# Kernel optimization log

Hardware: AMD Instinct MI355X
Metric: run time of the kernel (lower is better)

The kernel has to match this reference:

```python
import jax, jax.numpy as jnp
import numpy as np
import math

B = 16; L = 1024; CIN = 3; COUT = 1; D = 128; K = 16; DEPTH = 4
EPS = 1e-5; GRID_RANGE = 1.0


def _haar_basis(L):
    # Orthonormal Haar wavelet basis, rows of V (L, L). L must be power of 2.
    V = np.zeros((L, L), dtype=np.float64)
    V[0, :] = 1.0 / math.sqrt(L)
    r, s = 1, 1
    while s < L and r < L:
        block = 2 * s
        amp = 1.0 / math.sqrt(block)
        for j in range(L // block):
            st = j * block
            V[r, st:st + s] = amp
            V[r, st + s:st + block] = -amp
            r += 1
            if r >= L:
                break
        s *= 2
    return V


def _phi_f(L, k):
    # rFFT of top-k Haar basis rows, complex64 (matches build_stu_basis_rfft)
    V = _haar_basis(L)
    return jnp.asarray(np.fft.rfft(V, axis=-1)[:k].astype(np.complex64))


def setup_inputs() -> dict:
    key = jax.random.key(0)
    ks = jax.random.split(key, 8)

    def rn(k, shape, scale):
        return jax.random.normal(k, shape, dtype=jnp.float32) * scale

    return {
        "x": jax.random.normal(ks[0], (B, CIN, L), dtype=jnp.float32),
        "lift_w": rn(ks[1], (D, CIN + 1), 1.0 / math.sqrt(CIN + 1)),  # conv1x1 weight
        "lift_b": jnp.zeros((D,), jnp.float32),
        "Phi_f": _phi_f(L, K),                                        # (K, L//2+1) complex64 buffer
        "theta": rn(ks[2], (DEPTH, K, D, D), 1.0 / math.sqrt(D)),
        "ln_g": jnp.ones((DEPTH, D), jnp.float32),
        "ln_b": jnp.zeros((DEPTH, D), jnp.float32),
        "fc1_w": rn(ks[3], (DEPTH, 2 * D, D), 1.0 / math.sqrt(D)),
        "fc1_b": jnp.zeros((DEPTH, 2 * D), jnp.float32),
        "fc2_w": rn(ks[4], (DEPTH, D, 2 * D), 1.0 / math.sqrt(2 * D)),
        "fc2_b": jnp.zeros((DEPTH, D), jnp.float32),
        "head_w": rn(ks[5], (COUT, D), 1.0 / math.sqrt(D)),
        "head_b": jnp.zeros((COUT,), jnp.float32),
    }


def _forward(x, lift_w, lift_b, Phi_f, theta, ln_g, ln_b,
             fc1_w, fc1_b, fc2_w, fc2_b, head_w, head_b):
    # add_grid: append linspace coord channel -> (B, CIN+1, L)
    coords = jnp.linspace(0.0, GRID_RANGE, L, dtype=x.dtype)
    coords = jnp.broadcast_to(coords, (x.shape[0], 1, L))
    xg = jnp.concatenate([x, coords], axis=1)

    # LocalLift1D with kernel_size=1 == pointwise linear over channels
    h = jnp.einsum('bcl,dc->bdl', xg, lift_w) + lift_b[None, :, None]

    Phic = jnp.conj(Phi_f)  # (K, Lr)
    for i in range(DEPTH):
        # LayerNorm over channel dim (torch LN on transposed (B,L,D))
        mu = jnp.mean(h, axis=1, keepdims=True)
        var = jnp.var(h, axis=1, keepdims=True)
        z = (h - mu) / jnp.sqrt(var + EPS) * ln_g[i][None, :, None] + ln_b[i][None, :, None]

        Xf = jnp.fft.rfft(z, axis=-1)                       # (B, D, Lr)
        Uf = Xf[:, :, None, :] * Phic[None, None, :, :]     # (B, D, K, Lr)
        U = jnp.fft.irfft(Uf, n=L, axis=-1)                 # (B, D, K, L)

        # fused einsum('bdln,lhd->bhln') + sum over l(=k)
        S = jnp.einsum('bdkn,khd->bhn', U, theta[i])        # (B, D, L)

        # pointwise MLP (conv1x1 -> GELU -> conv1x1), residual
        H1 = jax.nn.gelu(jnp.einsum('bdl,hd->bhl', S, fc1_w[i]) + fc1_b[i][None, :, None],
                         approximate=False)
        h = h + jnp.einsum('bhl,dh->bdl', H1, fc2_w[i]) + fc2_b[i][None, :, None]

    # head: conv1x1 lifting_dim -> out_dim
    return jnp.einsum('bdl,od->bol', h, head_w) + head_b[None, :, None]


def reference(x, lift_w, lift_b, Phi_f, theta, ln_g, ln_b,
              fc1_w, fc1_b, fc2_w, fc2_b, head_w, head_b):
    return _forward(x, lift_w, lift_b, Phi_f, theta, ln_g, ln_b,
                    fc1_w, fc1_b, fc2_w, fc2_b, head_w, head_b)
```

## Files before the change

### kernel.cpp

```cpp
#include <hip/hip_runtime.h>
#include <math.h>

#define BB 16
#define LL 1024
#define DD 128
#define BL (BB*LL)
#define NDEPTH 4
#define EPSF 1e-5f

typedef unsigned short u16;
typedef short bf16x8 __attribute__((ext_vector_type(8)));
typedef short bf16x4 __attribute__((ext_vector_type(4)));
typedef float f32x4 __attribute__((ext_vector_type(4)));

static __device__ __forceinline__ u16 f2bf(float x) {
    unsigned u = __float_as_uint(x);
    u = u + 0x7fffu + ((u >> 16) & 1u);
    return (u16)(u >> 16);
}

#define DZ_B 0
#define S_B  15360
#define H1_B 23552
#define RST_B 39936
#define MRS_B 40064
#define LDS_TOT 40192

#define N_TH (4*15*16384)
#define N_W1 (4*32768)
#define N_W2 (4*32768)
__global__ __launch_bounds__(256) void cvt_kernel(const float* __restrict__ theta,
        const float* __restrict__ fc1w, const float* __restrict__ fc2w,
        u16* __restrict__ thf, u16* __restrict__ w1f, u16* __restrict__ w2f) {
    int o = blockIdx.x * 256 + threadIdx.x;
    if (o < N_TH) {
        int j = o & 7, ln = (o >> 3) & 63, c = (o >> 9) & 3, f = (o >> 11) & 7;
        int slab = o >> 14;
        int layer = slab / 15, kk = slab - layer * 15;
        int h = f * 16 + (ln & 15), d = 32 * c + 8 * (ln >> 4) + j;
        thf[o] = f2bf(theta[(((size_t)layer * 16 + kk + 1) * 128 + h) * 128 + d]);
    } else if (o < N_TH + N_W1) {
        int o2 = o - N_TH;
        int j = o2 & 7, ln = (o2 >> 3) & 63, c = (o2 >> 9) & 3, f = (o2 >> 11) & 15;
        int layer = o2 >> 15;
        int m = f * 16 + (ln & 15), d = 32 * c + 8 * (ln >> 4) + j;
        w1f[o2] = f2bf(fc1w[(size_t)layer * 32768 + m * 128 + d]);
    } else if (o < N_TH + N_W1 + N_W2) {
        int o2 = o - (N_TH + N_W1);
        int j = o2 & 7, ln = (o2 >> 3) & 63, c = (o2 >> 9) & 7, f = (o2 >> 12) & 7;
        int layer = o2 >> 15;
        int d = f * 16 + (ln & 15), m = 32 * c + 8 * (ln >> 4) + j;
        w2f[o2] = f2bf(fc2w[(size_t)layer * 32768 + d * 256 + m]);
    }
}

__global__ __launch_bounds__(512) void prep0_kernel(const float* __restrict__ x,
        const float* __restrict__ lw, const float* __restrict__ lb,
        float* __restrict__ H, float2* __restrict__ stats,
        float* __restrict__ P1p, float* __restrict__ P2p) {
    __shared__ char lds[16384 + 256];
    float* rst = (float*)(lds + 16384);
    float* mrs = (float*)(lds + 16384 + 128);
    int b = blockIdx.y, nblk = blockIdx.x, t0 = nblk * 32, tid = threadIdx.x;

    #pragma unroll
    for (int it = 0; it < 2; ++it) {
        int idx = it * 512 + tid;
        int r = idx >> 5, d0 = (idx & 31) * 4;
        int l = t0 + r;
        float x0 = x[(size_t)b * 3072 + l];
        float x1 = x[(size_t)b * 3072 + 1024 + l];
        float x2 = x[(size_t)b * 3072 + 2048 + l];
        float coord = (float)l * (1.0f / 1023.0f);
        f32x4 hv;
        #pragma unroll
        for (int q = 0; q < 4; ++q) {
            int d = d0 + q;
            float4 w = *(const float4*)(lw + d * 4);
            hv[q] = lb[d] + w.x * x0 + w.y * x1 + w.z * x2 + w.w * coord;
        }
        *(f32x4*)(H + ((size_t)b * 1024 + l) * 128 + d0) = hv;
        int byte = r * 512 + ((d0 * 4) ^ ((r & 7) << 4));
        *(f32x4*)(lds + byte) = hv;
    }
    __syncthreads();
    {
        int t = tid >> 4, q = tid & 15;
        float s = 0.f, sq = 0.f;
        #pragma unroll
        for (int dd = 0; dd < 8; dd += 4) {
            int d = q * 8 + dd;
            int byte = t * 512 + ((d * 4) ^ ((t & 7) << 4));
            f32x4 v = *(const f32x4*)(lds + byte);
            s += v[0] + v[1] + v[2] + v[3];
            sq += v[0]*v[0] + v[1]*v[1] + v[2]*v[2] + v[3]*v[3];
        }
        #pragma unroll
        for (int o = 1; o < 16; o <<= 1) {
            s += __shfl_xor(s, o, 64); sq += __shfl_xor(sq, o, 64);
        }
        if (q == 0) {
            float mu = s * (1.f / 128.f);
            float var = sq * (1.f / 128.f) - mu * mu;
            float rs = rsqrtf(var + EPSF);
            stats[(size_t)b * 1024 + t0 + t] = make_float2(mu, rs);
            rst[t] = rs; mrs[t] = mu * rs;
        }
    }
    __syncthreads();
    if (tid < 128) {
        float s = 0.f;
        #pragma unroll 8
        for (int t = 0; t < 32; ++t) {
            int byte = t * 512 + ((tid * 4) ^ ((t & 7) << 4));
            s += *(const float*)(lds + byte) * rst[t];
        }
        P1p[((size_t)b * 32 + nblk) * 128 + tid] = s;
    } else if (tid == 128) {
        float s = 0.f;
        for (int t = 0; t < 32; ++t) s += mrs[t];
        P2p[b * 32 + nblk] = s;
    }
}

__global__ __launch_bounds__(128) void c_kernel(const float* __restrict__ theta0,
        const float* __restrict__ P1p, const float* __restrict__ P2p,
        const float* __restrict__ lng, const float* __restrict__ lnb,
        float* __restrict__ C) {
    __shared__ float zsum[128];
    int b = blockIdx.x, hc = blockIdx.y, tid = threadIdx.x;
    float s = 0.f;
    #pragma unroll 8
    for (int j = 0; j < 32; ++j) s += P1p[((size_t)b * 32 + j) * 128 + tid];
    float p2 = 0.f;
    #pragma unroll 8
    for (int j = 0; j < 32; ++j) p2 += P2p[b * 32 + j];
    zsum[tid] = lng[tid] * (s - p2) + 1024.0f * lnb[tid];
    __syncthreads();
    int h = hc * 16 + (tid >> 3), q = tid & 7;
    const float* th = theta0 + h * 128 + q * 16;
    float acc = 0.f;
    #pragma unroll
    for (int d = 0; d < 16; d += 4) {
        float4 tv = *(const float4*)(th + d);
        acc += tv.x * zsum[q*16 + d] + tv.y * zsum[q*16 + d + 1]
             + tv.z * zsum[q*16 + d + 2] + tv.w * zsum[q*16 + d + 3];
    }
    acc += __shfl_xor(acc, 1, 64);
    acc += __shfl_xor(acc, 2, 64);
    acc += __shfl_xor(acc, 4, 64);
    if (q == 0) C[b * 128 + h] = acc * (1.0f / 32.0f);
}

template<int LAST>
__global__ __launch_bounds__(512, 4) void mega_kernel(
        const float* __restrict__ Hin, const float2* __restrict__ stin,
        const float* __restrict__ lng,
        const u16* __restrict__ thf, const float* __restrict__ Cb_,
        const u16* __restrict__ w1f, const float* __restrict__ b1,
        const u16* __restrict__ w2f, const float* __restrict__ b2,
        float* __restrict__ Hout, float2* __restrict__ stout,
        float* __restrict__ P1p, float* __restrict__ P2p,
        const float* __restrict__ hwp, const float* __restrict__ hbp,
        float* __restrict__ out) {
    __shared__ char lds[LDS_TOT];
    int b = blockIdx.y, nblk = blockIdx.x, n0 = nblk * 32, tid = threadIdx.x;
    const float inv_s2 = 0.70710678118654752f;

    const float* Hb = Hin + (size_t)b * 1024 * 128;
    const float2* stb = stin + (size_t)b * 1024;
    for (int c = tid; c < 60 * 16; c += 512) {
        int r = c >> 4, d0 = (c & 15) * 8;
        int gr = (n0 + r) & 1023, g1 = (n0 + r + 1) & 1023;
        const float* ha = Hb + (size_t)gr * 128 + d0;
        const float* hc = Hb + (size_t)g1 * 128 + d0;
        float2 sa = stb[gr], sb = stb[g1];
        u16 tmp[8];
        #pragma unroll
        for (int j = 0; j < 8; ++j) {
            float za = (ha[j] - sa.x) * sa.y;
            float zc = (hc[j] - sb.x) * sb.y;
            tmp[j] = f2bf((za - zc) * inv_s2 * lng[d0 + j]);
        }
        int byte = r * 256 + ((d0 * 2) ^ ((r & 7) << 4));
        *(bf16x8*)(lds + byte) = *(bf16x8*)tmp;
    }
    __syncthreads();

    int wave = tid >> 6, lane = tid & 63;
    int lm = lane & 15, lk = (lane >> 4) * 8;
    int fb = (wave & 3) * 2;
    int tw0 = (wave >> 2) * 16;
    f32x4 zero4 = {0.f, 0.f, 0.f, 0.f};

    f32x4 accS[2] = {zero4, zero4};
    {
        const u16* thl = thf + (size_t)lane * 8;
        #pragma unroll 4
        for (int it = 0; it < 60; ++it) {
            int kk = it >> 2, c4 = it & 3;
            bf16x8 afr0 = *(const bf16x8*)(thl + ((size_t)((kk * 8 + fb + 0) * 4 + c4) << 9));
            bf16x8 afr1 = *(const bf16x8*)(thl + ((size_t)((kk * 8 + fb + 1) * 4 + c4) << 9));
            int trow = tw0 + lm + 2 * kk;
            int byte = trow * 256 + (((c4 * 32 + lk) * 2) ^ ((trow & 7) << 4));
            bf16x8 bfr = *(const bf16x8*)(lds + byte);
            accS[0] = __builtin_amdgcn_mfma_f32_16x16x32_bf16(afr0, bfr, accS[0], 0, 0, 0);
            accS[1] = __builtin_amdgcn_mfma_f32_16x16x32_bf16(afr1, bfr, accS[1], 0, 0, 0);
        }
    }

    {
        const float* Crow = Cb_ + b * 128;
        int tl = tw0 + lm;
        #pragma unroll
        for (int mt = 0; mt < 2; ++mt) {
            int h0 = (fb + mt) * 16 + (lane >> 4) * 4;
            f32x4 cv = *(const f32x4*)(Crow + h0);
            u16 o[4];
            #pragma unroll
            for (int r = 0; r < 4; ++r) o[r] = f2bf(accS[mt][r] + cv[r]);
            int byte = S_B + tl * 256 + ((h0 * 2) ^ ((tl & 7) << 4));
            *(bf16x4*)(lds + byte) = *(bf16x4*)o;
        }
    }
    __syncthreads();

    {
        f32x4 acc1[2][2];
        #pragma unroll
        for (int mt = 0; mt < 2; ++mt)
            #pragma unroll
            for (int nt = 0; nt < 2; ++nt) acc1[mt][nt] = zero4;
        const u16* w1l = w1f + (size_t)lane * 8;
        #pragma unroll
        for (int c4 = 0; c4 < 4; ++c4) {
            bf16x8 afr[2], bfr[2];
            #pragma unroll
            for (int mt = 0; mt < 2; ++mt)
                afr[mt] = *(const bf16x8*)(w1l + ((size_t)((wave * 2 + mt) * 4 + c4) << 9));
            #pragma unroll
            for (int nt = 0; nt < 2; ++nt) {
                int tl = nt * 16 + lm;
                int byte = S_B + tl * 256 + (((c4 * 32 + lk) * 2) ^ ((tl & 7) << 4));
                bfr[nt] = *(const bf16x8*)(lds + byte);
            }
            #pragma unroll
            for (int mt = 0; mt < 2; ++mt)
                #pragma unroll
                for (int nt = 0; nt < 2; ++nt)
                    acc1[mt][nt] = __builtin_amdgcn_mfma_f32_16x16x32_bf16(
                        afr[mt], bfr[nt], acc1[mt][nt], 0, 0, 0);
        }
        #pragma unroll
        for (int mt = 0; mt < 2; ++mt) {
            int mo = wave * 32 + mt * 16 + (lane >> 4) * 4;
            f32x4 bb4 = *(const f32x4*)(b1 + mo);
            #pragma unroll
            for (int nt = 0; nt < 2; ++nt) {
                int tl = nt * 16 + lm;
                u16 o[4];
                #pragma unroll
                for (int r = 0; r < 4; ++r) {
                    float xv = acc1[mt][nt][r] + bb4[r];
                    o[r] = f2bf(0.5f * xv * (1.0f + erff(xv * 0.70710678118654752f)));
                }
                int byte = H1_B + tl * 512 + ((mo * 2) ^ ((tl & 7) << 4));
                *(bf16x4*)(lds + byte) = *(bf16x4*)o;
            }
        }
    }
    __syncthreads();

    f32x4 acc2[2] = {zero4, zero4};
    {
        const u16* w2l = w2f + (size_t)lane * 8;
        #pragma unroll
        for (int c8 = 0; c8 < 8; ++c8) {
            bf16x8 afr = *(const bf16x8*)(w2l + ((size_t)(wave * 8 + c8) << 9));
            #pragma unroll
            for (int nt = 0; nt < 2; ++nt) {
                int tl = nt * 16 + lm;
                int byte = H1_B + tl * 512 + (((c8 * 32 + lk) * 2) ^ ((tl & 7) << 4));
                bf16x8 bfr = *(const bf16x8*)(lds + byte);
                acc2[nt] = __builtin_amdgcn_mfma_f32_16x16x32_bf16(afr, bfr, acc2[nt], 0, 0, 0);
            }
        }
    }
    __syncthreads();

    {
        int dbase = wave * 16 + (lane >> 4) * 4;
        #pragma unroll
        for (int nt = 0; nt < 2; ++nt) {
            int tl = nt * 16 + lm;
            int byte = H1_B + tl * 512 + ((dbase * 4) ^ ((tl & 7) << 4));
            *(f32x4*)(lds + byte) = acc2[nt];
        }
    }
    __syncthreads();

    {
        const float* Hrow = Hin + ((size_t)b * 1024 + n0) * 128;
        float* Horow = Hout + ((size_t)b * 1024 + n0) * 128;
        #pragma unroll
        for (int it = 0; it < 2; ++it) {
            int idx = it * 512 + tid;
            int r = idx >> 5, d0 = (idx & 31) * 4;
            int byte = H1_B + r * 512 + ((d0 * 4) ^ ((r & 7) << 4));
            f32x4 v = *(const f32x4*)(lds + byte);
            f32x4 bb = *(const f32x4*)(b2 + d0);
            f32x4 hv = *(const f32x4*)(Hrow + (size_t)r * 128 + d0);
            hv = hv + v + bb;
            if (LAST) {
                f32x4 wv = *(const f32x4*)(hwp + d0);
                float s = hv[0]*wv[0] + hv[1]*wv[1] + hv[2]*wv[2] + hv[3]*wv[3];
                #pragma unroll
                for (int o = 1; o < 32; o <<= 1) s += __shfl_xor(s, o, 64);
                if ((lane & 31) == 0) out[(size_t)b * 1024 + n0 + r] = s + hbp[0];
            } else {
                *(f32x4*)(Horow + (size_t)r * 128 + d0) = hv;
                *(f32x4*)(lds + byte) = hv;
            }
        }
    }
    if (!LAST) {
        __syncthreads();
        float* rst = (float*)(lds + RST_B);
        float* mrs = (float*)(lds + MRS_B);
        {
            int t = tid >> 4, q = tid & 15;
            float s = 0.f, sq = 0.f;
            #pragma unroll
            for (int dd = 0; dd < 8; dd += 4) {
                int d = q * 8 + dd;
                int byte = H1_B + t * 512 + ((d * 4) ^ ((t & 7) << 4));
                f32x4 v = *(const f32x4*)(lds + byte);
                s += v[0] + v[1] + v[2] + v[3];
                sq += v[0]*v[0] + v[1]*v[1] + v[2]*v[2] + v[3]*v[3];
            }
            #pragma unroll
            for (int o = 1; o < 16; o <<= 1) {
                s += __shfl_xor(s, o, 64); sq += __shfl_xor(sq, o, 64);
            }
            if (q == 0) {
                float mu = s * (1.f / 128.f);
                float var = sq * (1.f / 128.f) - mu * mu;
                float rs = rsqrtf(var + EPSF);
                stout[(size_t)b * 1024 + n0 + t] = make_float2(mu, rs);
                rst[t] = rs; mrs[t] = mu * rs;
            }
        }
        __syncthreads();
        if (tid < 128) {
            float s = 0.f;
            #pragma unroll 8
            for (int t = 0; t < 32; ++t) {
                int byte = H1_B + t * 512 + ((tid * 4) ^ ((t & 7) << 4));
                s += *(const float*)(lds + byte) * rst[t];
            }
            P1p[((size_t)b * 32 + nblk) * 128 + tid] = s;
        } else if (tid == 128) {
            float s = 0.f;
            for (int t = 0; t < 32; ++t) s += mrs[t];
            P2p[b * 32 + nblk] = s;
        }
    }
}

extern "C" void kernel_launch(void* const* d_in, const int* in_sizes, int n_in,
                              void* d_out, int out_size, void* d_ws, size_t ws_size,
                              hipStream_t stream) {
    const float* x     = (const float*)d_in[0];
    const float* lw    = (const float*)d_in[1];
    const float* lb    = (const float*)d_in[2];
    const float* theta = (const float*)d_in[4];
    const float* ln_g  = (const float*)d_in[5];
    const float* ln_b  = (const float*)d_in[6];
    const float* fc1w  = (const float*)d_in[7];
    const float* fc1b  = (const float*)d_in[8];
    const float* fc2w  = (const float*)d_in[9];
    const float* fc2b  = (const float*)d_in[10];
    const float* hw    = (const float*)d_in[11];
    const float* hb    = (const float*)d_in[12];

    float* ws = (float*)d_ws;
    float* H_A = ws;
    float* H_B = H_A + (size_t)BL * DD;
    float2* st_A = (float2*)(H_B + (size_t)BL * DD);
    float2* st_B = st_A + BL;
    float* P1p = (float*)(st_B + BL);
    float* P2p = P1p + 16 * 32 * 128;
    float* Cb  = P2p + 512;
    u16* thf = (u16*)(Cb + 2048);
    u16* w1f = thf + N_TH;
    u16* w2f = w1f + N_W1;

    cvt_kernel<<<(N_TH + N_W1 + N_W2) / 256, 256, 0, stream>>>(theta, fc1w, fc2w, thf, w1f, w2f);
    prep0_kernel<<<dim3(32, 16), 512, 0, stream>>>(x, lw, lb, H_A, st_A, P1p, P2p);

    float* Hi = H_A; float* Ho = H_B;
    float2* sti = st_A; float2* sto = st_B;
    for (int i = 0; i < NDEPTH; ++i) {
        c_kernel<<<dim3(16, 8), 128, 0, stream>>>(theta + (size_t)i * 16 * 16384, P1p, P2p,
                                                  ln_g + i * 128, ln_b + i * 128, Cb);
        if (i < NDEPTH - 1) {
            mega_kernel<0><<<dim3(32, 16), 512, 0, stream>>>(
                Hi, sti, ln_g + i * 128,
                thf + (size_t)i * 15 * 16384, Cb,
                w1f + (size_t)i * 32768, fc1b + i * 256,
                w2f + (size_t)i * 32768, fc2b + i * 128,
                Ho, sto, P1p, P2p, hw, hb, (float*)d_out);
        } else {
            mega_kernel<1><<<dim3(32, 16), 512, 0, stream>>>(
                Hi, sti, ln_g + i * 128,
                thf + (size_t)i * 15 * 16384, Cb,
                w1f + (size_t)i * 32768, fc1b + i * 256,
                w2f + (size_t)i * 32768, fc2b + i * 128,
                Ho, sto, P1p, P2p, hw, hb, (float*)d_out);
        }
        float* tH = Hi; Hi = Ho; Ho = tH;
        float2* tS = sti; sti = sto; sto = tS;
    }
}
```

Before: 141.0 us.

## Fuse per-layer C bias kernel into mega kernel and restructure theta MFMA loop

Removes the separate c_kernel launch per layer. Each mega_kernel block now reduces the P1/P2 partials itself and computes the k=0 theta bias vector into LDS, using a bf16 copy of theta0 made in cvt_kernel. To avoid a read/write race, the P1/P2 partial buffers are double-buffered across layers. The spectral MFMA loop is also remapped so each wave owns 16 output channels across both 16-token tiles, with theta fragments double-buffered in registers. The cost is redundant C computation in every block and a bf16 rounding of theta0.

```diff
diff --git a/kernel.cpp b/kernel.cpp
--- a/kernel.cpp
+++ b/kernel.cpp
@@ -18,20 +18,27 @@
     u = u + 0x7fffu + ((u >> 16) & 1u);
     return (u16)(u >> 16);
 }
-
-#define DZ_B 0
-#define S_B  15360
-#define H1_B 23552
-#define RST_B 39936
-#define MRS_B 40064
-#define LDS_TOT 40192
+static __device__ __forceinline__ float bf2f(short v) {
+    return __uint_as_float(((unsigned)(unsigned short)v) << 16);
+}
+
+#define DZ_B  0
+#define S_B   15360
+#define H1_B  23552
+#define ZS_B  39936
+#define C_B   40448
+#define RST_B 40960
+#define MRS_B 41088
+#define LDS_TOT 41216
 
 #define N_TH (4*15*16384)
 #define N_W1 (4*32768)
 #define N_W2 (4*32768)
+#define N_TH0 (4*16384)
 __global__ __launch_bounds__(256) void cvt_kernel(const float* __restrict__ theta,
         const float* __restrict__ fc1w, const float* __restrict__ fc2w,
-        u16* __restrict__ thf, u16* __restrict__ w1f, u16* __restrict__ w2f) {
+        u16* __restrict__ thf, u16* __restrict__ w1f, u16* __restrict__ w2f,
+        u16* __restrict__ th0f) {
     int o = blockIdx.x * 256 + threadIdx.x;
     if (o < N_TH) {
         int j = o & 7, ln = (o >> 3) & 63, c = (o >> 9) & 3, f = (o >> 11) & 7;
@@ -51,6 +58,10 @@
         int layer = o2 >> 15;
         int d = f * 16 + (ln & 15), m = 32 * c + 8 * (ln >> 4) + j;
         w2f[o2] = f2bf(fc2w[(size_t)layer * 32768 + d * 256 + m]);
+    } else if (o < N_TH + N_W1 + N_W2 + N_TH0) {
+        int o2 = o - (N_TH + N_W1 + N_W2);
+        int layer = o2 >> 14, idx = o2 & 16383;
+        th0f[o2] = f2bf(theta[(size_t)layer * 262144 + idx]);
     }
 }
 
@@ -123,44 +134,16 @@
     }
 }
 
-__global__ __launch_bounds__(128) void c_kernel(const float* __restrict__ theta0,
-        const float* __restrict__ P1p, const float* __restrict__ P2p,
-        const float* __restrict__ lng, const float* __restrict__ lnb,
-        float* __restrict__ C) {
-    __shared__ float zsum[128];
-    int b = blockIdx.x, hc = blockIdx.y, tid = threadIdx.x;
-    float s = 0.f;
-    #pragma unroll 8
-    for (int j = 0; j < 32; ++j) s += P1p[((size_t)b * 32 + j) * 128 + tid];
-    float p2 = 0.f;
-    #pragma unroll 8
-    for (int j = 0; j < 32; ++j) p2 += P2p[b * 32 + j];
-    zsum[tid] = lng[tid] * (s - p2) + 1024.0f * lnb[tid];
-    __syncthreads();
-    int h = hc * 16 + (tid >> 3), q = tid & 7;
-    const float* th = theta0 + h * 128 + q * 16;
-    float acc = 0.f;
-    #pragma unroll
-    for (int d = 0; d < 16; d += 4) {
-        float4 tv = *(const float4*)(th + d);
-        acc += tv.x * zsum[q*16 + d] + tv.y * zsum[q*16 + d + 1]
-             + tv.z * zsum[q*16 + d + 2] + tv.w * zsum[q*16 + d + 3];
-    }
-    acc += __shfl_xor(acc, 1, 64);
-    acc += __shfl_xor(acc, 2, 64);
-    acc += __shfl_xor(acc, 4, 64);
-    if (q == 0) C[b * 128 + h] = acc * (1.0f / 32.0f);
-}
-
 template<int LAST>
 __global__ __launch_bounds__(512, 4) void mega_kernel(
         const float* __restrict__ Hin, const float2* __restrict__ stin,
-        const float* __restrict__ lng,
-        const u16* __restrict__ thf, const float* __restrict__ Cb_,
+        const float* __restrict__ lng, const float* __restrict__ lnb,
+        const u16* __restrict__ thf, const u16* __restrict__ th0f,
         const u16* __restrict__ w1f, const float* __restrict__ b1,
         const u16* __restrict__ w2f, const float* __restrict__ b2,
         float* __restrict__ Hout, float2* __restrict__ stout,
-        float* __restrict__ P1p, float* __restrict__ P2p,
+        const float* __restrict__ P1in, const float* __restrict__ P2in,
+        float* __restrict__ P1out, float* __restrict__ P2out,
         const float* __restrict__ hwp, const float* __restrict__ hbp,
         float* __restrict__ out) {
     __shared__ char lds[LDS_TOT];
@@ -185,40 +168,96 @@
         int byte = r * 256 + ((d0 * 2) ^ ((r & 7) << 4));
         *(bf16x8*)(lds + byte) = *(bf16x8*)tmp;
     }
+    if (tid < 128) {
+        float s = 0.f;
+        #pragma unroll 8
+        for (int j = 0; j < 32; ++j) s += P1in[((size_t)b * 32 + j) * 128 + tid];
+        float p2 = 0.f;
+        #pragma unroll 8
+        for (int j = 0; j < 32; ++j) p2 += P2in[b * 32 + j];
+        ((float*)(lds + ZS_B))[tid] = lng[tid] * (s - p2) + 1024.0f * lnb[tid];
+    }
     __syncthreads();
 
     int wave = tid >> 6, lane = tid & 63;
     int lm = lane & 15, lk = (lane >> 4) * 8;
-    int fb = (wave & 3) * 2;
-    int tw0 = (wave >> 2) * 16;
     f32x4 zero4 = {0.f, 0.f, 0.f, 0.f};
 
+    {
+        int h = tid >> 2, q = tid & 3;
+        const u16* th0 = th0f + h * 128 + q * 32;
+        const float* zs = (const float*)(lds + ZS_B) + q * 32;
+        float acc = 0.f;
+        #pragma unroll
+        for (int c = 0; c < 4; ++c) {
+            bf16x8 tv = *(const bf16x8*)(th0 + c * 8);
+            #pragma unroll
+            for (int j = 0; j < 8; ++j) acc += bf2f(tv[j]) * zs[c * 8 + j];
+        }
+        acc += __shfl_xor(acc, 1, 64);
+        acc += __shfl_xor(acc, 2, 64);
+        if (q == 0) ((float*)(lds + C_B))[h] = acc * (1.0f / 32.0f);
+    }
+    __syncthreads();
+
     f32x4 accS[2] = {zero4, zero4};
     {
-        const u16* thl = thf + (size_t)lane * 8;
-        #pragma unroll 4
-        for (int it = 0; it < 60; ++it) {
-            int kk = it >> 2, c4 = it & 3;
-            bf16x8 afr0 = *(const bf16x8*)(thl + ((size_t)((kk * 8 + fb + 0) * 4 + c4) << 9));
-            bf16x8 afr1 = *(const bf16x8*)(thl + ((size_t)((kk * 8 + fb + 1) * 4 + c4) << 9));
-            int trow = tw0 + lm + 2 * kk;
-            int byte = trow * 256 + (((c4 * 32 + lk) * 2) ^ ((trow & 7) << 4));
-            bf16x8 bfr = *(const bf16x8*)(lds + byte);
-            accS[0] = __builtin_amdgcn_mfma_f32_16x16x32_bf16(afr0, bfr, accS[0], 0, 0, 0);
-            accS[1] = __builtin_amdgcn_mfma_f32_16x16x32_bf16(afr1, bfr, accS[1], 0, 0, 0);
-        }
-    }
-
-    {
-        const float* Crow = Cb_ + b * 128;
-        int tl = tw0 + lm;
-        #pragma unroll
-        for (int mt = 0; mt < 2; ++mt) {
-            int h0 = (fb + mt) * 16 + (lane >> 4) * 4;
-            f32x4 cv = *(const f32x4*)(Crow + h0);
+        const u16* thl = thf + (size_t)lane * 8 + (size_t)wave * 2048;
+        bf16x8 bufA[4], bufB[4];
+        #pragma unroll
+        for (int c4 = 0; c4 < 4; ++c4)
+            bufA[c4] = *(const bf16x8*)(thl + c4 * 512);
+        #pragma unroll
+        for (int kp = 0; kp < 7; ++kp) {
+            int kk = kp * 2;
+            #pragma unroll
+            for (int c4 = 0; c4 < 4; ++c4)
+                bufB[c4] = *(const bf16x8*)(thl + (size_t)(kk + 1) * 16384 + c4 * 512);
+            #pragma unroll
+            for (int c4 = 0; c4 < 4; ++c4) {
+                #pragma unroll
+                for (int nt = 0; nt < 2; ++nt) {
+                    int trow = nt * 16 + lm + 2 * kk;
+                    int byte = trow * 256 + (((c4 * 32 + lk) * 2) ^ ((trow & 7) << 4));
+                    bf16x8 bfr = *(const bf16x8*)(lds + byte);
+                    accS[nt] = __builtin_amdgcn_mfma_f32_16x16x32_bf16(bufA[c4], bfr, accS[nt], 0, 0, 0);
+                }
+            }
+            #pragma unroll
+            for (int c4 = 0; c4 < 4; ++c4)
+                bufA[c4] = *(const bf16x8*)(thl + (size_t)(kk + 2) * 16384 + c4 * 512);
+            #pragma unroll
+            for (int c4 = 0; c4 < 4; ++c4) {
+                #pragma unroll
+                for (int nt = 0; nt < 2; ++nt) {
+                    int trow = nt * 16 + lm + 2 * (kk + 1);
+                    int byte = trow * 256 + (((c4 * 32 + lk) * 2) ^ ((trow & 7) << 4));
+                    bf16x8 bfr = *(const bf16x8*)(lds + byte);
+                    accS[nt] = __builtin_amdgcn_mfma_f32_16x16x32_bf16(bufB[c4], bfr, accS[nt], 0, 0, 0);
+                }
+            }
+        }
+        #pragma unroll
+        for (int c4 = 0; c4 < 4; ++c4) {
+            #pragma unroll
+            for (int nt = 0; nt < 2; ++nt) {
+                int trow = nt * 16 + lm + 28;
+                int byte = trow * 256 + (((c4 * 32 + lk) * 2) ^ ((trow & 7) << 4));
+                bf16x8 bfr = *(const bf16x8*)(lds + byte);
+                accS[nt] = __builtin_amdgcn_mfma_f32_16x16x32_bf16(bufA[c4], bfr, accS[nt], 0, 0, 0);
+            }
+        }
+    }
+
+    {
+        int h0 = wave * 16 + (lane >> 4) * 4;
+        f32x4 cv = *(const f32x4*)(lds + C_B + h0 * 4);
+        #pragma unroll
+        for (int nt = 0; nt < 2; ++nt) {
+            int tl = nt * 16 + lm;
             u16 o[4];
             #pragma unroll
-            for (int r = 0; r < 4; ++r) o[r] = f2bf(accS[mt][r] + cv[r]);
+            for (int r = 0; r < 4; ++r) o[r] = f2bf(accS[nt][r] + cv[r]);
             int byte = S_B + tl * 256 + ((h0 * 2) ^ ((tl & 7) << 4));
             *(bf16x4*)(lds + byte) = *(bf16x4*)o;
         }
@@ -358,11 +397,11 @@
                 int byte = H1_B + t * 512 + ((tid * 4) ^ ((t & 7) << 4));
                 s += *(const float*)(lds + byte) * rst[t];
             }
-            P1p[((size_t)b * 32 + nblk) * 128 + tid] = s;
+            P1out[((size_t)b * 32 + nblk) * 128 + tid] = s;
         } else if (tid == 128) {
             float s = 0.f;
             for (int t = 0; t < 32; ++t) s += mrs[t];
-            P2p[b * 32 + nblk] = s;
+            P2out[b * 32 + nblk] = s;
         }
     }
 }
@@ -388,37 +427,43 @@
     float* H_B = H_A + (size_t)BL * DD;
     float2* st_A = (float2*)(H_B + (size_t)BL * DD);
     float2* st_B = st_A + BL;
-    float* P1p = (float*)(st_B + BL);
-    float* P2p = P1p + 16 * 32 * 128;
-    float* Cb  = P2p + 512;
-    u16* thf = (u16*)(Cb + 2048);
-    u16* w1f = thf + N_TH;
-    u16* w2f = w1f + N_W1;
-
-    cvt_kernel<<<(N_TH + N_W1 + N_W2) / 256, 256, 0, stream>>>(theta, fc1w, fc2w, thf, w1f, w2f);
-    prep0_kernel<<<dim3(32, 16), 512, 0, stream>>>(x, lw, lb, H_A, st_A, P1p, P2p);
+    float* P1A = (float*)(st_B + BL);
+    float* P1B = P1A + 16 * 32 * 128;
+    float* P2A = P1B + 16 * 32 * 128;
+    float* P2B = P2A + 512;
+    u16* thf  = (u16*)(P2B + 512);
+    u16* w1f  = thf + N_TH;
+    u16* w2f  = w1f + N_W1;
+    u16* th0f = w2f + N_W2;
+
+    cvt_kernel<<<(N_TH + N_W1 + N_W2 + N_TH0) / 256, 256, 0, stream>>>(
+        theta, fc1w, fc2w, thf, w1f, w2f, th0f);
+    prep0_kernel<<<dim3(32, 16), 512, 0, stream>>>(x, lw, lb, H_A, st_A, P1A, P2A);
 
     float* Hi = H_A; float* Ho = H_B;
     float2* sti = st_A; float2* sto = st_B;
+    float* p1i = P1A; float* p1o = P1B;
+    float* p2i = P2A; float* p2o = P2B;
     for (int i = 0; i < NDEPTH; ++i) {
-        c_kernel<<<dim3(16, 8), 128, 0, stream>>>(theta + (size_t)i * 16 * 16384, P1p, P2p,
-                                                  ln_g + i * 128, ln_b + i * 128, Cb);
         if (i < NDEPTH - 1) {
             mega_kernel<0><<<dim3(32, 16), 512, 0, stream>>>(
-                Hi, sti, ln_g + i * 128,
-                thf + (size_t)i * 15 * 16384, Cb,
+                Hi, sti, ln_g + i * 128, ln_b + i * 128,
+                thf + (size_t)i * 15 * 16384, th0f + (size_t)i * 16384,
                 w1f + (size_t)i * 32768, fc1b + i * 256,
                 w2f + (size_t)i * 32768, fc2b + i * 128,
-                Ho, sto, P1p, P2p, hw, hb, (float*)d_out);
+                Ho, sto, p1i, p2i, p1o, p2o, hw, hb, (float*)d_out);
         } else {
             mega_kernel<1><<<dim3(32, 16), 512, 0, stream>>>(
-                Hi, sti, ln_g + i * 128,
-                thf + (size_t)i * 15 * 16384, Cb,
+                Hi, sti, ln_g + i * 128, ln_b + i * 128,
+                thf + (size_t)i * 15 * 16384, th0f + (size_t)i * 16384,
                 w1f + (size_t)i * 32768, fc1b + i * 256,
                 w2f + (size_t)i * 32768, fc2b + i * 128,
-                Ho, sto, P1p, P2p, hw, hb, (float*)d_out);
-        }
-        float* tH = Hi; Hi = Ho; Ho = tH;
-        float2* tS = sti; sti = sto; sto = tS;
-    }
-}
+                Ho, sto, p1i, p2i, p1o, p2o, hw, hb, (float*)d_out);
+        }
+        float* t;
+        t = Hi; Hi = Ho; Ho = t;
+        float2* ts = sti; sti = sto; sto = ts;
+        t = p1i; p1i = p1o; p1o = t;
+        t = p2i; p2i = p2o; p2o = t;
+    }
+}
```

Measured after the change: 148.2 us. 5.1% more time.
